# Kernel optimization log

Measured on AMD Instinct MI355X. Metric: run time of the kernel, lower is better.

## Reference

```python
import jax, jax.numpy as jnp
import numpy as np

LN_EPS = 1e-5


def setup_inputs() -> dict:
    key = jax.random.key(0)
    k1, k2, k3, k4 = jax.random.split(key, 4)
    B, S, F, H = 128, 1024, 16, 512
    x = jax.random.normal(k1, (B, S, F), dtype=jnp.float32)
    # stacked per-feature Linear(1,H): W[i] = feature_projs[i].weight[:,0], b[i] = bias
    W = jax.random.normal(k2, (F, H), dtype=jnp.float32) * (1.0 / np.sqrt(F))
    b = jax.random.normal(k3, (F, H), dtype=jnp.float32) * 0.02
    emb = jax.random.normal(k4, (S, H), dtype=jnp.float32)  # num_stabilizers == S
    gamma = jnp.ones((H,), dtype=jnp.float32)
    beta = jnp.zeros((H,), dtype=jnp.float32)
    return {"x": x, "W": W, "b": b, "emb": emb, "gamma": gamma, "beta": beta}


def reference(x, W, b, emb, gamma, beta):
    # sum_i Linear_i(x[...,i:i+1]) == x @ W + sum_i b_i  (single fused GEMM)
    h = jnp.einsum("bsf,fh->bsh", x, W) + b.sum(axis=0)
    # index embedding: idx = arange(S), broadcast over batch
    h = h + emb[: x.shape[1]]  # (B,S,H) + (S,H)
    # LayerNorm over last dim
    mu = h.mean(axis=-1, keepdims=True)
    var = h.var(axis=-1, keepdims=True)
    hn = (h - mu) * jax.lax.rsqrt(var + LN_EPS)
    return hn * gamma + beta
```

## Files before the change

kernel.cpp:

```cpp
#include <hip/hip_runtime.h>

#define LN_EPS 1e-5f

static constexpr int Hc  = 512;
static constexpr int Fc  = 16;
static constexpr int Sc  = 1024;
static constexpr int Bc  = 128;
static constexpr int RPW = 16;

__global__ void bsum_kernel(const float* __restrict__ b, float* __restrict__ bsum) {
    int h = blockIdx.x * 64 + threadIdx.x;
    float s = 0.f;
#pragma unroll
    for (int i = 0; i < Fc; ++i) s += b[i * Hc + h];
    bsum[h] = s;
}

template <int CTRL, int RMASK>
__device__ __forceinline__ float dpp_add(float v) {
    int t = __builtin_amdgcn_update_dpp(0, __float_as_int(v), CTRL, RMASK, 0xf, true);
    return v + __int_as_float(t);
}
__device__ __forceinline__ float wave_sum64(float v) {
    v = dpp_add<0x111, 0xf>(v);
    v = dpp_add<0x112, 0xf>(v);
    v = dpp_add<0x114, 0xf>(v);
    v = dpp_add<0x118, 0xf>(v);
    v = dpp_add<0x142, 0xa>(v);
    v = dpp_add<0x143, 0xc>(v);
    return __int_as_float(__builtin_amdgcn_readlane(__float_as_int(v), 63));
}

__device__ __forceinline__ float rdlane(float v, int l) {
    return __int_as_float(__builtin_amdgcn_readlane(__float_as_int(v), l));
}

__global__ __launch_bounds__(256) void fused_kernel(
    const float* __restrict__ x, const float* __restrict__ W,
    const float* __restrict__ emb, const float* __restrict__ bsum,
    const float* __restrict__ gamma, const float* __restrict__ beta,
    float* __restrict__ out)
{
    const int lane = threadIdx.x & 63;
    const int wid  = (blockIdx.x << 2) | (threadIdx.x >> 6);
    const int s    = wid & (Sc - 1);
    const int g    = wid >> 10;
    const int h0 = lane * 4, h1 = h0 + 256;

    float4 w0[Fc], w1[Fc];
#pragma unroll
    for (int i = 0; i < Fc; ++i) {
        w0[i] = *reinterpret_cast<const float4*>(&W[i * Hc + h0]);
        w1[i] = *reinterpret_cast<const float4*>(&W[i * Hc + h1]);
    }

    const int sub = lane >> 4, i16 = lane & 15;
    float xq0, xq1, xq2, xq3;
    {
        const size_t xoff = (size_t)s * Fc + i16;
        xq0 = __builtin_nontemporal_load(&x[(size_t)(g * 16 + 0 * 4 + sub) * Sc * Fc + xoff]);
        xq1 = __builtin_nontemporal_load(&x[(size_t)(g * 16 + 1 * 4 + sub) * Sc * Fc + xoff]);
        xq2 = __builtin_nontemporal_load(&x[(size_t)(g * 16 + 2 * 4 + sub) * Sc * Fc + xoff]);
        xq3 = __builtin_nontemporal_load(&x[(size_t)(g * 16 + 3 * 4 + sub) * Sc * Fc + xoff]);
    }

    const float4 g0  = *reinterpret_cast<const float4*>(&gamma[h0]);
    const float4 g1  = *reinterpret_cast<const float4*>(&gamma[h1]);
    const float4 be0 = *reinterpret_cast<const float4*>(&beta[h0]);
    const float4 be1 = *reinterpret_cast<const float4*>(&beta[h1]);
    float4 ebs0, ebs1;
    {
        const float4 e0  = *reinterpret_cast<const float4*>(&emb[(size_t)s * Hc + h0]);
        const float4 e1  = *reinterpret_cast<const float4*>(&emb[(size_t)s * Hc + h1]);
        const float4 bs0 = *reinterpret_cast<const float4*>(&bsum[h0]);
        const float4 bs1 = *reinterpret_cast<const float4*>(&bsum[h1]);
        ebs0.x = e0.x + bs0.x; ebs0.y = e0.y + bs0.y; ebs0.z = e0.z + bs0.z; ebs0.w = e0.w + bs0.w;
        ebs1.x = e1.x + bs1.x; ebs1.y = e1.y + bs1.y; ebs1.z = e1.z + bs1.z; ebs1.w = e1.w + bs1.w;
    }

#pragma unroll
    for (int t = 0; t < RPW; ++t) {
        const float xsrc = (t >> 2) == 0 ? xq0 : (t >> 2) == 1 ? xq1 : (t >> 2) == 2 ? xq2 : xq3;
        float xs[Fc];
#pragma unroll
        for (int i = 0; i < Fc; ++i)
            xs[i] = rdlane(xsrc, (t & 3) * 16 + i);

        float4 a0 = ebs0, a1 = ebs1;
#pragma unroll
        for (int i = 0; i < Fc; ++i) {
            a0.x = fmaf(xs[i], w0[i].x, a0.x);
            a0.y = fmaf(xs[i], w0[i].y, a0.y);
            a0.z = fmaf(xs[i], w0[i].z, a0.z);
            a0.w = fmaf(xs[i], w0[i].w, a0.w);
            a1.x = fmaf(xs[i], w1[i].x, a1.x);
            a1.y = fmaf(xs[i], w1[i].y, a1.y);
            a1.z = fmaf(xs[i], w1[i].z, a1.z);
            a1.w = fmaf(xs[i], w1[i].w, a1.w);
        }

        float psum = a0.x + a0.y + a0.z + a0.w + a1.x + a1.y + a1.z + a1.w;
        float pssq = fmaf(a0.x, a0.x, fmaf(a0.y, a0.y, fmaf(a0.z, a0.z, a0.w * a0.w)));
        pssq = fmaf(a1.x, a1.x, fmaf(a1.y, a1.y, fmaf(a1.z, a1.z, fmaf(a1.w, a1.w, pssq))));

        const float sum = wave_sum64(psum);
        const float ssq = wave_sum64(pssq);

        const float mean = sum * (1.0f / 512.0f);
        const float var  = ssq * (1.0f / 512.0f) - mean * mean;
        const float rs   = rsqrtf(var + LN_EPS);

        float4 r0, r1;
        r0.x = (a0.x - mean) * rs * g0.x + be0.x;
        r0.y = (a0.y - mean) * rs * g0.y + be0.y;
        r0.z = (a0.z - mean) * rs * g0.z + be0.z;
        r0.w = (a0.w - mean) * rs * g0.w + be0.w;
        r1.x = (a1.x - mean) * rs * g1.x + be1.x;
        r1.y = (a1.y - mean) * rs * g1.y + be1.y;
        r1.z = (a1.z - mean) * rs * g1.z + be1.z;
        r1.w = (a1.w - mean) * rs * g1.w + be1.w;

        float* orow = out + ((size_t)(g * 16 + t) * Sc + s) * Hc;
        *reinterpret_cast<float4*>(&orow[h0]) = r0;
        *reinterpret_cast<float4*>(&orow[h1]) = r1;
    }
}

extern "C" void kernel_launch(void* const* d_in, const int* in_sizes, int n_in,
                              void* d_out, int out_size, void* d_ws, size_t ws_size,
                              hipStream_t stream) {
    const float* x     = (const float*)d_in[0];
    const float* W     = (const float*)d_in[1];
    const float* b     = (const float*)d_in[2];
    const float* emb   = (const float*)d_in[3];
    const float* gamma = (const float*)d_in[4];
    const float* beta  = (const float*)d_in[5];
    float* out  = (float*)d_out;
    float* bsum = (float*)d_ws;

    bsum_kernel<<<Hc / 64, 64, 0, stream>>>(b, bsum);

    const int blocks = (8 * Sc) / 4;
    fused_kernel<<<blocks, 256, 0, stream>>>(x, W, emb, bsum, gamma, beta, out);
}
```

Measured before the change: 70.86 us.

## Split each LayerNorm row across two waves with LDS partial-sum exchange

Each row of 512 outputs is now handled by two waves, each covering 256 columns, instead of one wave covering all 512. This halves the per-thread W register footprint and doubles the block count, aiming for higher occupancy and more memory-level parallelism on this store-bound kernel. The cost is an LDS exchange of partial sums plus a block-wide barrier on every row iteration, using double-buffered shared slots.

```diff
diff --git a/kernel.cpp b/kernel.cpp
--- a/kernel.cpp
+++ b/kernel.cpp
@@ -5,7 +5,6 @@
 static constexpr int Hc  = 512;
 static constexpr int Fc  = 16;
 static constexpr int Sc  = 1024;
-static constexpr int Bc  = 128;
 static constexpr int RPW = 16;
 
 __global__ void bsum_kernel(const float* __restrict__ b, float* __restrict__ bsum) {
@@ -41,41 +40,38 @@
     const float* __restrict__ gamma, const float* __restrict__ beta,
     float* __restrict__ out)
 {
-    const int lane = threadIdx.x & 63;
-    const int wid  = (blockIdx.x << 2) | (threadIdx.x >> 6);
-    const int s    = wid & (Sc - 1);
-    const int g    = wid >> 10;
-    const int h0 = lane * 4, h1 = h0 + 256;
+    __shared__ float2 part[2][4];
 
-    float4 w0[Fc], w1[Fc];
+    const int lane  = threadIdx.x & 63;
+    const int wv    = threadIdx.x >> 6;
+    const int half  = wv & 1;
+    const int p     = blockIdx.x * 2 + (wv >> 1);
+    const int s     = p & (Sc - 1);
+    const int g     = p >> 10;
+    const int h     = half * 256 + lane * 4;
+
+    float4 Wp[Fc];
 #pragma unroll
-    for (int i = 0; i < Fc; ++i) {
-        w0[i] = *reinterpret_cast<const float4*>(&W[i * Hc + h0]);
-        w1[i] = *reinterpret_cast<const float4*>(&W[i * Hc + h1]);
-    }
+    for (int i = 0; i < Fc; ++i)
+        Wp[i] = *reinterpret_cast<const float4*>(&W[i * Hc + h]);
 
     const int sub = lane >> 4, i16 = lane & 15;
     float xq0, xq1, xq2, xq3;
     {
         const size_t xoff = (size_t)s * Fc + i16;
-        xq0 = __builtin_nontemporal_load(&x[(size_t)(g * 16 + 0 * 4 + sub) * Sc * Fc + xoff]);
-        xq1 = __builtin_nontemporal_load(&x[(size_t)(g * 16 + 1 * 4 + sub) * Sc * Fc + xoff]);
-        xq2 = __builtin_nontemporal_load(&x[(size_t)(g * 16 + 2 * 4 + sub) * Sc * Fc + xoff]);
-        xq3 = __builtin_nontemporal_load(&x[(size_t)(g * 16 + 3 * 4 + sub) * Sc * Fc + xoff]);
+        xq0 = __builtin_nontemporal_load(&x[(size_t)(g * 16 +  0 + sub) * Sc * Fc + xoff]);
+        xq1 = __builtin_nontemporal_load(&x[(size_t)(g * 16 +  4 + sub) * Sc * Fc + xoff]);
+        xq2 = __builtin_nontemporal_load(&x[(size_t)(g * 16 +  8 + sub) * Sc * Fc + xoff]);
+        xq3 = __builtin_nontemporal_load(&x[(size_t)(g * 16 + 12 + sub) * Sc * Fc + xoff]);
     }
 
-    const float4 g0  = *reinterpret_cast<const float4*>(&gamma[h0]);
-    const float4 g1  = *reinterpret_cast<const float4*>(&gamma[h1]);
-    const float4 be0 = *reinterpret_cast<const float4*>(&beta[h0]);
-    const float4 be1 = *reinterpret_cast<const float4*>(&beta[h1]);
-    float4 ebs0, ebs1;
+    const float4 gmv = *reinterpret_cast<const float4*>(&gamma[h]);
+    const float4 bev = *reinterpret_cast<const float4*>(&beta[h]);
+    float4 ebs;
     {
-        const float4 e0  = *reinterpret_cast<const float4*>(&emb[(size_t)s * Hc + h0]);
-        const float4 e1  = *reinterpret_cast<const float4*>(&emb[(size_t)s * Hc + h1]);
-        const float4 bs0 = *reinterpret_cast<const float4*>(&bsum[h0]);
-        const float4 bs1 = *reinterpret_cast<const float4*>(&bsum[h1]);
-        ebs0.x = e0.x + bs0.x; ebs0.y = e0.y + bs0.y; ebs0.z = e0.z + bs0.z; ebs0.w = e0.w + bs0.w;
-        ebs1.x = e1.x + bs1.x; ebs1.y = e1.y + bs1.y; ebs1.z = e1.z + bs1.z; ebs1.w = e1.w + bs1.w;
+        const float4 e  = *reinterpret_cast<const float4*>(&emb[(size_t)s * Hc + h]);
+        const float4 bs = *reinterpret_cast<const float4*>(&bsum[h]);
+        ebs.x = e.x + bs.x; ebs.y = e.y + bs.y; ebs.z = e.z + bs.z; ebs.w = e.w + bs.w;
     }
 
 #pragma unroll
@@ -86,43 +82,38 @@
         for (int i = 0; i < Fc; ++i)
             xs[i] = rdlane(xsrc, (t & 3) * 16 + i);
 
-        float4 a0 = ebs0, a1 = ebs1;
+        float4 a = ebs;
 #pragma unroll
         for (int i = 0; i < Fc; ++i) {
-            a0.x = fmaf(xs[i], w0[i].x, a0.x);
-            a0.y = fmaf(xs[i], w0[i].y, a0.y);
-            a0.z = fmaf(xs[i], w0[i].z, a0.z);
-            a0.w = fmaf(xs[i], w0[i].w, a0.w);
-            a1.x = fmaf(xs[i], w1[i].x, a1.x);
-            a1.y = fmaf(xs[i], w1[i].y, a1.y);
-            a1.z = fmaf(xs[i], w1[i].z, a1.z);
-            a1.w = fmaf(xs[i], w1[i].w, a1.w);
+            a.x = fmaf(xs[i], Wp[i].x, a.x);
+            a.y = fmaf(xs[i], Wp[i].y, a.y);
+            a.z = fmaf(xs[i], Wp[i].z, a.z);
+            a.w = fmaf(xs[i], Wp[i].w, a.w);
         }
 
-        float psum = a0.x + a0.y + a0.z + a0.w + a1.x + a1.y + a1.z + a1.w;
-        float pssq = fmaf(a0.x, a0.x, fmaf(a0.y, a0.y, fmaf(a0.z, a0.z, a0.w * a0.w)));
-        pssq = fmaf(a1.x, a1.x, fmaf(a1.y, a1.y, fmaf(a1.z, a1.z, fmaf(a1.w, a1.w, pssq))));
+        float psum = a.x + a.y + a.z + a.w;
+        float pssq = fmaf(a.x, a.x, fmaf(a.y, a.y, fmaf(a.z, a.z, a.w * a.w)));
 
-        const float sum = wave_sum64(psum);
-        const float ssq = wave_sum64(pssq);
+        float sum = wave_sum64(psum);
+        float ssq = wave_sum64(pssq);
+
+        if (lane == 0) part[t & 1][wv] = make_float2(sum, ssq);
+        asm volatile("s_waitcnt lgkmcnt(0)" ::: "memory");
+        __builtin_amdgcn_s_barrier();
+        asm volatile("" ::: "memory");
+        const float2 o = part[t & 1][wv ^ 1];
+        sum += o.x; ssq += o.y;
 
         const float mean = sum * (1.0f / 512.0f);
         const float var  = ssq * (1.0f / 512.0f) - mean * mean;
         const float rs   = rsqrtf(var + LN_EPS);
 
-        float4 r0, r1;
-        r0.x = (a0.x - mean) * rs * g0.x + be0.x;
-        r0.y = (a0.y - mean) * rs * g0.y + be0.y;
-        r0.z = (a0.z - mean) * rs * g0.z + be0.z;
-        r0.w = (a0.w - mean) * rs * g0.w + be0.w;
-        r1.x = (a1.x - mean) * rs * g1.x + be1.x;
-        r1.y = (a1.y - mean) * rs * g1.y + be1.y;
-        r1.z = (a1.z - mean) * rs * g1.z + be1.z;
-        r1.w = (a1.w - mean) * rs * g1.w + be1.w;
-
-        float* orow = out + ((size_t)(g * 16 + t) * Sc + s) * Hc;
-        *reinterpret_cast<float4*>(&orow[h0]) = r0;
-        *reinterpret_cast<float4*>(&orow[h1]) = r1;
+        float4 r;
+        r.x = (a.x - mean) * rs * gmv.x + bev.x;
+        r.y = (a.y - mean) * rs * gmv.y + bev.y;
+        r.z = (a.z - mean) * rs * gmv.z + bev.z;
+        r.w = (a.w - mean) * rs * gmv.w + bev.w;
+        *reinterpret_cast<float4*>(&out[((size_t)(g * 16 + t) * Sc + s) * Hc + h]) = r;
     }
 }
 
@@ -140,6 +131,6 @@
 
     bsum_kernel<<<Hc / 64, 64, 0, stream>>>(b, bsum);
 
-    const int blocks = (8 * Sc) / 4;
+    const int blocks = (8 * Sc) / 2;
     fused_kernel<<<blocks, 256, 0, stream>>>(x, W, emb, bsum, gamma, beta, out);
 }
```

New measurement: 77.58 us. 9.5% more time.
